# Kernel tuning notes

Measured on AMD Instinct MI355X. Metric: run time of the kernel, lower is better.

## Reference

```python
import jax, jax.numpy as jnp
import numpy as np
from jax import lax

NPOINTS = 1024
K = 32
EPS = 1e-5


def fps(xyz, npoints):
    # Furthest point sampling. xyz: (B, N, 3) -> idx (B, npoints) int32.
    B, N, _ = xyz.shape
    def step(carry, _):
        dists, last = carry
        last_xyz = jnp.take_along_axis(xyz, last[:, None, None], axis=1)  # (B,1,3)
        d = jnp.sum((xyz - last_xyz) ** 2, axis=-1)  # (B,N)
        dists = jnp.minimum(dists, d)
        nxt = jnp.argmax(dists, axis=-1).astype(jnp.int32)
        return (dists, nxt), last
    init = (jnp.full((B, N), 1e10, xyz.dtype), jnp.zeros((B,), jnp.int32))
    _, idx = lax.scan(step, init, None, length=npoints)
    return idx.T  # (B, npoints)


def knn_idx(new_xyz, xyz, k):
    # new_xyz (B,S,3), xyz (B,N,3) -> (B,S,k) indices of k nearest neighbors.
    d = (jnp.sum(new_xyz ** 2, -1)[:, :, None]
         - 2.0 * jnp.einsum('bsc,bnc->bsn', new_xyz, xyz)
         + jnp.sum(xyz ** 2, -1)[:, None, :])  # (B,S,N)
    _, idx = lax.top_k(-d, k)
    return idx


def batch_gather(x, idx):
    # x (B, N, C), idx (B, ...) -> (B, ..., C)
    return jax.vmap(lambda a, i: a[i])(x, idx)


def bn(x, g, b, axes):
    # training-mode batchnorm over `axes`, channel on last axis
    m = jnp.mean(x, axes, keepdims=True)
    v = jnp.var(x, axes, keepdims=True)
    return g * (x - m) * lax.rsqrt(v + EPS) + b


def setup_inputs() -> dict:
    key = jax.random.key(0)
    ks = jax.random.split(key, 8)
    B, N, D, Cw, OUT = 16, 4096, 64, 64, 64
    inp = {
        'xyz': jax.random.uniform(ks[0], (B, N, 3), jnp.float32),
        'feature': jax.random.normal(ks[1], (B, D, N), jnp.float32),
        'w0': jax.random.normal(ks[2], (3, Cw), jnp.float32) * 0.3,
        'b0': jnp.zeros((Cw,), jnp.float32),
        'g0': jnp.ones((Cw,), jnp.float32),
        'be0': jnp.zeros((Cw,), jnp.float32),
        'w1': jax.random.normal(ks[3], (Cw, Cw), jnp.float32) * 0.1,
        'b1': jnp.zeros((Cw,), jnp.float32),
        'g1': jnp.ones((Cw,), jnp.float32),
        'be1': jnp.zeros((Cw,), jnp.float32),
        'w2': jax.random.normal(ks[4], (Cw, Cw), jnp.float32) * 0.1,
        'b2': jnp.zeros((Cw,), jnp.float32),
        'g2': jnp.ones((Cw,), jnp.float32),
        'be2': jnp.zeros((Cw,), jnp.float32),
        'wf': jax.random.normal(ks[5], (D * Cw, OUT), jnp.float32) * 0.02,
        'bf': jnp.zeros((OUT,), jnp.float32),
        'gf': jnp.ones((OUT,), jnp.float32),
        'bef': jnp.zeros((OUT,), jnp.float32),
    }
    return inp


def reference(xyz, feature, w0, b0, g0, be0, w1, b1, g1, be1, w2, b2, g2, be2, wf, bf, gf, bef):
    B, N, _ = xyz.shape
    # FPS + gather centroids
    fps_idx = fps(xyz, NPOINTS)                    # (B, S)
    new_xyz = batch_gather(xyz, fps_idx)           # (B, S, 3)
    # kNN grouping
    idx = knn_idx(new_xyz, xyz, K)                 # (B, S, K)
    grouped_xyz = batch_gather(xyz, idx) - new_xyz[:, :, None, :]   # (B,S,K,3)
    feat_nlast = jnp.swapaxes(feature, 1, 2)       # (B, N, D)
    grouped_feature = batch_gather(feat_nlast, idx)  # (B, S, K, D)
    # WeightNet: 1x1 conv MLP 3 -> Cw -> Cw -> Cw with BN+ReLU
    h = grouped_xyz
    for w, b, g, be in ((w0, b0, g0, be0), (w1, b1, g1, be1), (w2, b2, g2, be2)):
        h = jax.nn.relu(bn(h @ w + b, g, be, (0, 1, 2)))  # (B,S,K,Cw)
    weights = h
    # per-centroid matmul: (B,S,D,K) x (B,S,K,Cw) -> (B,S,D,Cw)
    nf = jnp.einsum('bskd,bskw->bsdw', grouped_feature, weights)
    nf = nf.reshape(B, NPOINTS, -1)                # (B, S, D*Cw)
    # final Conv1d(1x1) + BN1d + ReLU
    out = jax.nn.relu(bn(nf @ wf + bf, gf, bef, (0, 1)))  # (B, S, OUT)
    out = jnp.swapaxes(out, 1, 2)                  # (B, OUT, S)
    return (new_xyz, out)
```

## Files before the change

### kernel.cpp

```cpp
#include <hip/hip_runtime.h>

#define NBATCH 16
#define NPTS   4096
#define NSAMP  1024
#define NKNN   32
#define NROWS  (NBATCH*NSAMP*NKNN)
#define BN_EPS 1e-5f
#define H1PAD  66
#define KNN_CAP 512

typedef __attribute__((ext_vector_type(4))) float f32x4;
typedef __attribute__((ext_vector_type(8))) short bf16x8;
union frag_u { unsigned u[4]; bf16x8 h; uint4 u4; };

__device__ __forceinline__ unsigned pack_bf16pair(float a, float b) {
    unsigned ua = __float_as_uint(a); ua += 0x7FFFu + ((ua >> 16) & 1u);
    unsigned ub = __float_as_uint(b); ub += 0x7FFFu + ((ub >> 16) & 1u);
    return (ua >> 16) | (ub & 0xFFFF0000u);
}

__global__ __launch_bounds__(256) void fps_kernel(const float* __restrict__ xyz,
                                                  float* __restrict__ newxyz)
{
    const int b = blockIdx.x;
    const int tid = threadIdx.x;
    const int wv = tid >> 6;
    const float* xb = xyz + (size_t)b * NPTS * 3;
    __shared__ float xs[NPTS];
    __shared__ float ys[NPTS];
    __shared__ float zs[NPTS];
    __shared__ __align__(16) float4 red[2][4];
    __shared__ __align__(16) float nxs[NSAMP*3];
    float px[16], py[16], pz[16], dmin[16];
    {
        float arr[48];
        const float4* s4 = (const float4*)(xb + (size_t)tid * 48);
        #pragma unroll
        for (int i = 0; i < 12; ++i) *(float4*)&arr[i*4] = s4[i];
        #pragma unroll
        for (int j = 0; j < 16; ++j) {
            px[j] = arr[3*j]; py[j] = arr[3*j+1]; pz[j] = arr[3*j+2];
            const int p = tid * 16 + j;
            xs[p] = px[j]; ys[p] = py[j]; zs[p] = pz[j];
            dmin[j] = 1e10f;
        }
    }
    if (tid == 0) { nxs[0] = xb[0]; nxs[1] = xb[1]; nxs[2] = xb[2]; }
    __syncthreads();
    float lx = xs[0], ly = ys[0], lz = zs[0];
    for (int t = 1; t < NSAMP; ++t) {
        float bv = -1.0f;
        #pragma unroll
        for (int j = 0; j < 16; ++j) {
            const float dx = __fsub_rn(px[j], lx);
            const float dy = __fsub_rn(py[j], ly);
            const float dz = __fsub_rn(pz[j], lz);
            const float d = __fadd_rn(__fadd_rn(__fmul_rn(dx,dx), __fmul_rn(dy,dy)), __fmul_rn(dz,dz));
            const float nd = fminf(dmin[j], d);
            dmin[j] = nd;
            bv = fmaxf(bv, nd);
        }
        int lj = 0;
        #pragma unroll
        for (int j = 15; j >= 0; --j) if (dmin[j] == bv) lj = j;
        const int bi_lane = tid * 16 + lj;
        float mv = bv;
        {
            int s_;
            s_ = __builtin_amdgcn_mov_dpp(__float_as_int(mv), 0x111, 0xf, 0xf, true);
            mv = fmaxf(mv, __int_as_float(s_));
            s_ = __builtin_amdgcn_mov_dpp(__float_as_int(mv), 0x112, 0xf, 0xf, true);
            mv = fmaxf(mv, __int_as_float(s_));
            s_ = __builtin_amdgcn_mov_dpp(__float_as_int(mv), 0x114, 0xf, 0xf, true);
            mv = fmaxf(mv, __int_as_float(s_));
            s_ = __builtin_amdgcn_mov_dpp(__float_as_int(mv), 0x118, 0xf, 0xf, true);
            mv = fmaxf(mv, __int_as_float(s_));
            s_ = __builtin_amdgcn_mov_dpp(__float_as_int(mv), 0x142, 0xf, 0xf, true);
            mv = fmaxf(mv, __int_as_float(s_));
            s_ = __builtin_amdgcn_mov_dpp(__float_as_int(mv), 0x143, 0xf, 0xf, true);
            mv = fmaxf(mv, __int_as_float(s_));
        }
        mv = __int_as_float(__builtin_amdgcn_readlane(__float_as_int(mv), 63));
        const unsigned long long mask = __ballot(bv == mv);
        const int winner = __ffsll(mask) - 1;
        const int bi_w = __builtin_amdgcn_readlane(bi_lane, winner);
        const float wx = xs[bi_w], wy = ys[bi_w], wz = zs[bi_w];
        const int par = t & 1;
        if ((tid & 63) == 0) red[par][wv] = make_float4(mv, wx, wy, wz);
        __syncthreads();
        float4 w0 = red[par][0];
        const float4 w1 = red[par][1];
        const float4 w2 = red[par][2];
        const float4 w3 = red[par][3];
        if (w1.x > w0.x) w0 = w1;
        if (w2.x > w0.x) w0 = w2;
        if (w3.x > w0.x) w0 = w3;
        lx = w0.y; ly = w0.z; lz = w0.w;
        if (tid == 0) { nxs[t*3] = lx; nxs[t*3+1] = ly; nxs[t*3+2] = lz; }
    }
    __syncthreads();
    {
        float4* d4 = (float4*)(newxyz + (size_t)b * NSAMP * 3);
        const float4* s4 = (const float4*)nxs;
        #pragma unroll
        for (int i = tid; i < NSAMP*3/4; i += 256) d4[i] = s4[i];
    }
}

__device__ __forceinline__ void bin_select(int* hist, int* ctrl, int* wsum,
                                           int tid, int shift)
{
    const int lane = tid & 63, wv = tid >> 6;
    const int cnt = hist[tid];
    const int r = ctrl[1];
    int incl = cnt;
    #pragma unroll
    for (int d = 1; d < 64; d <<= 1) {
        const int v = __shfl_up(incl, d);
        if (lane >= d) incl += v;
    }
    if (lane == 63) wsum[wv] = incl;
    __syncthreads();
    int base = 0;
    if (wv > 0) base += wsum[0];
    if (wv > 1) base += wsum[1];
    if (wv > 2) base += wsum[2];
    incl += base;
    const int excl = incl - cnt;
    if (excl < r && r <= incl) {
        ctrl[0] |= tid << shift;
        ctrl[1] = r - excl;
        ctrl[2] = cnt;
    }
}

__global__ __launch_bounds__(256) void knn_kernel(const float* __restrict__ xyz,
                                                  const float* __restrict__ newxyz,
                                                  int* __restrict__ idx_out)
{
    const int bs = blockIdx.x;
    const int b = bs >> 10;
    const int tid = threadIdx.x;
    __shared__ unsigned keys[NPTS];
    __shared__ int hist[256];
    __shared__ float qsh[3];
    __shared__ int ctrl[8];
    __shared__ int wsum[4];
    __shared__ int cl[KNN_CAP];
    __shared__ int lt[32];
    __shared__ int ties[128];
    if (tid < 3) qsh[tid] = newxyz[bs*3 + tid];
    if (tid == 0) { ctrl[0] = 0; ctrl[1] = NKNN; }
    hist[tid] = 0;
    __syncthreads();
    const float q0 = qsh[0], q1 = qsh[1], q2 = qsh[2];
    const float qq = __fadd_rn(__fadd_rn(__fmul_rn(q0,q0), __fmul_rn(q1,q1)), __fmul_rn(q2,q2));
    const float* xb = xyz + (size_t)b * NPTS * 3;
    for (int n = tid; n < NPTS; n += 256) {
        const float x0 = xb[n*3+0], x1 = xb[n*3+1], x2 = xb[n*3+2];
        const float xx = __fadd_rn(__fadd_rn(__fmul_rn(x0,x0), __fmul_rn(x1,x1)), __fmul_rn(x2,x2));
        float dt = __fmul_rn(q0, x0);
        dt = __fmaf_rn(q1, x1, dt);
        dt = __fmaf_rn(q2, x2, dt);
        const float dd = __fadd_rn(__fsub_rn(qq, __fmul_rn(2.0f, dt)), xx);
        unsigned ub = __float_as_uint(dd);
        ub = (ub & 0x80000000u) ? ~ub : (ub | 0x80000000u);
        keys[n] = ub;
        atomicAdd(&hist[ub >> 24], 1);
    }
    __syncthreads();
    bin_select(hist, ctrl, wsum, tid, 24);
    __syncthreads();
    const unsigned pf3 = (unsigned)ctrl[0];
    const int bin3 = (int)(pf3 >> 24);
    const int m = ctrl[2];
    const bool compact = (m <= KNN_CAP);
    if (tid == 0) { ctrl[3] = 0; ctrl[4] = 0; ctrl[5] = 0; ctrl[6] = 0; }
    __syncthreads();
    if (compact) {
        for (int n = tid; n < NPTS; n += 256) {
            const int tb = (int)(keys[n] >> 24);
            if (tb == bin3)      { const int pos = atomicAdd(&ctrl[3], 1); cl[pos] = n; }
            else if (tb < bin3)  { const int pos = atomicAdd(&ctrl[4], 1); lt[pos] = n; }
        }
    }
    __syncthreads();
    for (int p = 2; p >= 0; --p) {
        hist[tid] = 0;
        __syncthreads();
        const unsigned pre = (unsigned)ctrl[0];
        const int shift = p * 8;
        const unsigned himask = 0xFFFFFFFFu << ((p + 1) * 8);
        if (compact) {
            const int eqn = ctrl[3];
            for (int i = tid; i < eqn; i += 256) {
                const unsigned k = keys[cl[i]];
                if ((k & himask) == pre) atomicAdd(&hist[(k >> shift) & 255], 1);
            }
        } else {
            for (int n = tid; n < NPTS; n += 256) {
                const unsigned k = keys[n];
                if ((k & himask) == pre) atomicAdd(&hist[(k >> shift) & 255], 1);
            }
        }
        __syncthreads();
        bin_select(hist, ctrl, wsum, tid, shift);
        __syncthreads();
    }
    const unsigned T = (unsigned)ctrl[0];
    int* out = idx_out + (size_t)bs * NKNN;
    if (compact) {
        const int ltn = ctrl[4];
        if (tid == 0) ctrl[5] = ltn;
        __syncthreads();
        if (tid < ltn) out[tid] = lt[tid];
        const int eqn = ctrl[3];
        for (int i = tid; i < eqn; i += 256) {
            const int n = cl[i];
            const unsigned k = keys[n];
            if (k < T) {
                const int pos = atomicAdd(&ctrl[5], 1);
                if (pos < NKNN) out[pos] = n;
            } else if (k == T) {
                const int pos = atomicAdd(&ctrl[6], 1);
                if (pos < 128) ties[pos] = n;
            }
        }
    } else {
        for (int n = tid; n < NPTS; n += 256) {
            const unsigned k = keys[n];
            if (k < T) {
                const int pos = atomicAdd(&ctrl[5], 1);
                if (pos < NKNN) out[pos] = n;
            } else if (k == T) {
                const int pos = atomicAdd(&ctrl[6], 1);
                if (pos < 128) ties[pos] = n;
            }
        }
    }
    __syncthreads();
    if (tid == 0) {
        const int nless = ctrl[5] < NKNN ? ctrl[5] : NKNN;
        const int need = NKNN - nless;
        const int ntie = ctrl[6] < 128 ? ctrl[6] : 128;
        int last = -1;
        for (int j = 0; j < need; ++j) {
            int best = 0x7fffffff;
            for (int i = 0; i < ntie; ++i) {
                const int v = ties[i];
                if (v > last && v < best) best = v;
            }
            out[nless + j] = (best == 0x7fffffff) ? 0 : best;
            last = best;
        }
    }
}

__global__ void zero_all_kernel(double* st, float* g1, float* g2)
{
    const int i = blockIdx.x * 256 + threadIdx.x;
    if (i < 512) st[i] = 0.0;
    if (i < 4096) { g1[i] = 0.f; g2[i] = 0.f; }
}

__global__ __launch_bounds__(256) void gxmoments_kernel(
    const float* __restrict__ xyz, const float* __restrict__ newxyz,
    const int* __restrict__ idxws, double* __restrict__ stats)
{
    const int tid = threadIdx.x;
    float m[9];
    #pragma unroll
    for (int i = 0; i < 9; ++i) m[i] = 0.f;
    for (int row = blockIdx.x * 256 + tid; row < NROWS; row += gridDim.x * 256) {
        const int bs = row >> 5;
        const int bb = row >> 15;
        const int id = idxws[row];
        const float* xp = xyz + ((size_t)bb * NPTS + id) * 3;
        const float* qp = newxyz + bs * 3;
        const float dx = xp[0] - qp[0];
        const float dy = xp[1] - qp[1];
        const float dz = xp[2] - qp[2];
        m[0] += dx; m[1] += dy; m[2] += dz;
        m[3] += dx*dx; m[4] += dx*dy; m[5] += dx*dz;
        m[6] += dy*dy; m[7] += dy*dz; m[8] += dz*dz;
    }
    double d[9];
    #pragma unroll
    for (int i = 0; i < 9; ++i) {
        d[i] = (double)m[i];
        #pragma unroll
        for (int s = 1; s < 64; s <<= 1) d[i] += __shfl_xor(d[i], s);
    }
    __shared__ double part[4][9];
    if ((tid & 63) == 0) {
        #pragma unroll
        for (int i = 0; i < 9; ++i) part[tid >> 6][i] = d[i];
    }
    __syncthreads();
    if (tid < 9) atomicAdd(&stats[tid], part[0][tid] + part[1][tid] + part[2][tid] + part[3][tid]);
}

__global__ void bn0_moments_finalize_kernel(const double* __restrict__ st,
    const float* __restrict__ w0, const float* __restrict__ b0,
    const float* __restrict__ g0, const float* __restrict__ be0,
    float* __restrict__ outp)
{
    const int c = threadIdx.x;
    const double N = (double)NROWS;
    const double w0c = w0[c], w1c = w0[64 + c], w2c = w0[128 + c];
    const double b = b0[c];
    const double dotS = st[0]*w0c + st[1]*w1c + st[2]*w2c;
    const double qf = w0c*w0c*st[3] + w1c*w1c*st[6] + w2c*w2c*st[8]
                    + 2.0*(w0c*w1c*st[4] + w0c*w2c*st[5] + w1c*w2c*st[7]);
    const double mean = dotS / N + b;
    const double ex2 = (qf + 2.0*b*dotS) / N + b*b;
    const double var = ex2 - mean*mean;
    const float scale = g0[c] * rsqrtf((float)var + BN_EPS);
    outp[c] = scale;
    outp[64 + c] = be0[c] - (float)mean * scale;
}

__global__ void wfpack_all_kernel(const float* __restrict__ wf,
                                  const float* __restrict__ w1,
                                  const float* __restrict__ w2,
                                  unsigned* __restrict__ wfb,
                                  unsigned* __restrict__ w1b,
                                  unsigned* __restrict__ w2b)
{
    int blk = blockIdx.x;
    const float* src; unsigned* dst;
    if (blk < 512)      { src = wf; dst = wfb; }
    else if (blk < 520) { src = w1; dst = w1b; blk -= 512; }
    else                { src = w2; dst = w2b; blk -= 520; }
    const int kt = blk >> 2, ot = blk & 3;
    const int l = threadIdx.x;
    const int o = ot*16 + (l & 15);
    const int kb = kt*32 + (l >> 4)*8;
    unsigned out[4];
    #pragma unroll
    for (int r = 0; r < 4; ++r) {
        const float a = src[(size_t)(kb + 2*r) * 64 + o];
        const float b = src[(size_t)(kb + 2*r + 1) * 64 + o];
        out[r] = pack_bf16pair(a, b);
    }
    *(uint4*)&dst[((size_t)blk * 64 + l) * 4] = *(const uint4*)out;
}

__global__ __launch_bounds__(256) void gram1_kernel(
    const float* __restrict__ xyz, const float* __restrict__ newxyz,
    const int* __restrict__ idxws,
    const float* __restrict__ w0, const float* __restrict__ b0,
    const float* __restrict__ bnp, float* __restrict__ G1,
    double* __restrict__ Sh1)
{
    __shared__ float gxs[32][3];
    __shared__ float h1s[32][H1PAD];
    __shared__ float rsum[256];
    const int tid = threadIdx.x;
    const int c = tid & 63;
    const int rq = tid >> 6;
    const int lg = c >> 4, lm = c & 15;
    const float w0c0 = w0[c], w0c1 = w0[64+c], w0c2 = w0[128+c];
    const float b0c = b0[c], sc0 = bnp[c], sh0 = bnp[64+c];
    f32x4 Ga[4] = {{0,0,0,0},{0,0,0,0},{0,0,0,0},{0,0,0,0}};
    float sumh = 0.f;
    for (int chunk = blockIdx.x; chunk < NROWS/32; chunk += gridDim.x) {
        if (tid < 96) {
            const int slot = tid / 3, cc = tid % 3;
            const int row = chunk*32 + slot;
            const int bs = row >> 5, bb = row >> 15;
            gxs[slot][cc] = xyz[((size_t)bb * NPTS + idxws[row]) * 3 + cc] - newxyz[bs*3 + cc];
        }
        __syncthreads();
        #pragma unroll
        for (int i = 0; i < 8; ++i) {
            const int r = rq*8 + i;
            const float t0 = gxs[r][0]*w0c0 + gxs[r][1]*w0c1 + gxs[r][2]*w0c2 + b0c;
            const float h = fmaxf(sc0*t0 + sh0, 0.f);
            h1s[r][c] = h;
            sumh += h;
        }
        __syncthreads();
        frag_u fr[4];
        #pragma unroll
        for (int ct = 0; ct < 4; ++ct)
            #pragma unroll
            for (int r = 0; r < 4; ++r)
                fr[ct].u[r] = pack_bf16pair(h1s[lg*8 + 2*r][ct*16 + lm],
                                            h1s[lg*8 + 2*r + 1][ct*16 + lm]);
        #pragma unroll
        for (int ct = 0; ct < 4; ++ct)
            Ga[ct] = __builtin_amdgcn_mfma_f32_16x16x32_bf16(fr[rq].h, fr[ct].h, Ga[ct], 0, 0, 0);
        __syncthreads();
    }
    #pragma unroll
    for (int ct = 0; ct < 4; ++ct)
        #pragma unroll
        for (int r = 0; r < 4; ++r)
            atomicAdd(&G1[(rq*16 + lg*4 + r)*64 + ct*16 + lm], Ga[ct][r]);
    rsum[tid] = sumh;
    __syncthreads();
    if (tid < 64) atomicAdd(&Sh1[c], (double)(rsum[c] + rsum[64+c] + rsum[128+c] + rsum[192+c]));
}

__global__ __launch_bounds__(256) void gram2_kernel(
    const float* __restrict__ xyz, const float* __restrict__ newxyz,
    const int* __restrict__ idxws,
    const float* __restrict__ w0, const float* __restrict__ b0,
    const float* __restrict__ b1, const unsigned* __restrict__ w1b,
    const float* __restrict__ bnp, float* __restrict__ G2,
    double* __restrict__ Sh2)
{
    __shared__ float gxs[32][3];
    __shared__ float h1s[32][H1PAD];
    __shared__ float h2s[32][H1PAD];
    __shared__ float rsum[256];
    const int tid = threadIdx.x;
    const int c = tid & 63;
    const int rq = tid >> 6;
    const int lg = c >> 4, lm = c & 15;
    const int c2 = rq*16 + lm;
    const float w0c0 = w0[c], w0c1 = w0[64+c], w0c2 = w0[128+c];
    const float b0c = b0[c], sc0 = bnp[c], sh0 = bnp[64+c];
    const float b1c2 = b1[c2], sc1 = bnp[128+c2], sh1 = bnp[192+c2];
    frag_u Bw1[2];
    Bw1[0].u4 = *(const uint4*)&w1b[((0*4 + rq)*64 + c)*4];
    Bw1[1].u4 = *(const uint4*)&w1b[((1*4 + rq)*64 + c)*4];
    f32x4 Ga[4] = {{0,0,0,0},{0,0,0,0},{0,0,0,0},{0,0,0,0}};
    float sumh = 0.f;
    for (int chunk = blockIdx.x; chunk < NROWS/32; chunk += gridDim.x) {
        if (tid < 96) {
            const int slot = tid / 3, cc = tid % 3;
            const int row = chunk*32 + slot;
            const int bs = row >> 5, bb = row >> 15;
            gxs[slot][cc] = xyz[((size_t)bb * NPTS + idxws[row]) * 3 + cc] - newxyz[bs*3 + cc];
        }
        __syncthreads();
        #pragma unroll
        for (int i = 0; i < 8; ++i) {
            const int r = rq*8 + i;
            const float t0 = gxs[r][0]*w0c0 + gxs[r][1]*w0c1 + gxs[r][2]*w0c2 + b0c;
            h1s[r][c] = fmaxf(sc0*t0 + sh0, 0.f);
        }
        __syncthreads();
        #pragma unroll
        for (int mt = 0; mt < 2; ++mt) {
            f32x4 acc = {0,0,0,0};
            #pragma unroll
            for (int kt = 0; kt < 2; ++kt) {
                frag_u a;
                #pragma unroll
                for (int r = 0; r < 4; ++r) {
                    const float2 f = *(const float2*)&h1s[mt*16 + lm][kt*32 + lg*8 + 2*r];
                    a.u[r] = pack_bf16pair(f.x, f.y);
                }
                acc = __builtin_amdgcn_mfma_f32_16x16x32_bf16(a.h, Bw1[kt].h, acc, 0, 0, 0);
            }
            #pragma unroll
            for (int r = 0; r < 4; ++r)
                h2s[mt*16 + lg*4 + r][c2] = fmaxf(sc1*(acc[r] + b1c2) + sh1, 0.f);
        }
        __syncthreads();
        #pragma unroll
        for (int i = 0; i < 8; ++i) sumh += h2s[rq*8 + i][c];
        frag_u fr[4];
        #pragma unroll
        for (int ct = 0; ct < 4; ++ct)
            #pragma unroll
            for (int r = 0; r < 4; ++r)
                fr[ct].u[r] = pack_bf16pair(h2s[lg*8 + 2*r][ct*16 + lm],
                                            h2s[lg*8 + 2*r + 1][ct*16 + lm]);
        #pragma unroll
        for (int ct = 0; ct < 4; ++ct)
            Ga[ct] = __builtin_amdgcn_mfma_f32_16x16x32_bf16(fr[rq].h, fr[ct].h, Ga[ct], 0, 0, 0);
        __syncthreads();
    }
    #pragma unroll
    for (int ct = 0; ct < 4; ++ct)
        #pragma unroll
        for (int r = 0; r < 4; ++r)
            atomicAdd(&G2[(rq*16 + lg*4 + r)*64 + ct*16 + lm], Ga[ct][r]);
    rsum[tid] = sumh;
    __syncthreads();
    if (tid < 64) atomicAdd(&Sh2[c], (double)(rsum[c] + rsum[64+c] + rsum[128+c] + rsum[192+c]));
}

__global__ __launch_bounds__(256) void bn_gram_finalize_kernel(
    const double* __restrict__ Sh, const float* __restrict__ G,
    const float* __restrict__ w, const float* __restrict__ bias,
    const float* __restrict__ g, const float* __restrict__ be,
    float* __restrict__ outp)
{
    __shared__ float wls[64][65];
    __shared__ double shl[64];
    __shared__ double rd[256], rqd[256];
    const int tid = threadIdx.x;
    const int c = tid & 63;
    const int rqi = tid >> 6;
    for (int i = tid; i < 4096; i += 256) wls[i >> 6][i & 63] = w[i];
    if (tid < 64) shl[tid] = Sh[tid];
    __syncthreads();
    double dot = 0.0, quad = 0.0;
    for (int j = rqi*16; j < rqi*16 + 16; ++j) {
        const double wjc = (double)wls[j][c];
        dot += wjc * shl[j];
        double inner = 0.0;
        for (int k = 0; k < 64; ++k) inner += (double)G[j*64 + k] * (double)wls[k][c];
        quad += wjc * inner;
    }
    rd[tid] = dot; rqd[tid] = quad;
    __syncthreads();
    if (tid < 64) {
        const double d = rd[c] + rd[64+c] + rd[128+c] + rd[192+c];
        const double q = rqd[c] + rqd[64+c] + rqd[128+c] + rqd[192+c];
        const double N = (double)NROWS;
        const double bc = (double)bias[c];
        const double mean = d / N + bc;
        const double ex2 = (q + 2.0*bc*d) / N + bc*bc;
        const double var = ex2 - mean*mean;
        const float scale = g[c] * rsqrtf((float)var + BN_EPS);
        outp[c] = scale;
        outp[64 + c] = be[c] - (float)mean * scale;
    }
}

__global__ void bn_finalize_kernel(const double* __restrict__ st,
                                   const float* __restrict__ g,
                                   const float* __restrict__ be,
                                   float* __restrict__ outp, float n)
{
    const int c = threadIdx.x;
    const double m = st[c] / (double)n;
    const double var = st[64 + c] / (double)n - m * m;
    const float scale = g[c] * rsqrtf((float)var + BN_EPS);
    outp[c] = scale;
    outp[64 + c] = be[c] - (float)m * scale;
}

__global__ __launch_bounds__(256) void final_conv_kernel(
    const float* __restrict__ xyz, const float* __restrict__ newxyz,
    const int* __restrict__ idxws, const float* __restrict__ feat,
    const float* __restrict__ w0, const float* __restrict__ b0,
    const float* __restrict__ b1, const float* __restrict__ b2,
    const float* __restrict__ bnp, const unsigned* __restrict__ wfb,
    const unsigned* __restrict__ w1b, const unsigned* __restrict__ w2b,
    const float* __restrict__ bf, float* __restrict__ y)
{
    __shared__ unsigned wtp[8][16][64];
    __shared__ __align__(16) float scratch[2*64*H1PAD];
    __shared__ float gxs[256][3];
    __shared__ int   idxs[8][32];
    __shared__ float qs[8][3];
    float* h1s = scratch;
    float* h2s = scratch + 64*H1PAD;
    unsigned* yaf = (unsigned*)scratch;
    const int tid = threadIdx.x;
    const int c = tid & 63;
    const int rq = tid >> 6;
    const int lg = c >> 4, lm = c & 15;
    const int c2 = rq*16 + lm;
    const int bs0 = blockIdx.x * 8;
    const int b = bs0 >> 10;
    idxs[tid >> 5][tid & 31] = idxws[(size_t)bs0 * NKNN + tid];
    if (tid < 24)  qs[tid / 3][tid % 3] = newxyz[(bs0 + tid/3)*3 + (tid % 3)];
    const float w0c0 = w0[c], w0c1 = w0[64+c], w0c2 = w0[128+c];
    const float b0c = b0[c], sc0 = bnp[c], sh0 = bnp[64+c];
    const float b1c2 = b1[c2], sc1 = bnp[128+c2], sh1 = bnp[192+c2];
    const float b2c2 = b2[c2], sc2 = bnp[256+c2], sh2 = bnp[320+c2];
    frag_u Bw1[2], Bw2[2];
    #pragma unroll
    for (int kt = 0; kt < 2; ++kt) {
        Bw1[kt].u4 = *(const uint4*)&w1b[((kt*4 + rq)*64 + c)*4];
        Bw2[kt].u4 = *(const uint4*)&w2b[((kt*4 + rq)*64 + c)*4];
    }
    __syncthreads();
    for (int i = tid; i < 768; i += 256) {
        const int row = i / 3, cc = i - row * 3;
        const int e = row >> 5, k = row & 31;
        gxs[row][cc] = xyz[((size_t)b * NPTS + idxs[e][k]) * 3 + cc] - qs[e][cc];
    }
    __syncthreads();
    for (int chunk = 0; chunk < 4; ++chunk) {
        #pragma unroll
        for (int i = 0; i < 16; ++i) {
            const int r = rq*16 + i;
            const int gr = chunk*64 + r;
            const float t0 = gxs[gr][0]*w0c0 + gxs[gr][1]*w0c1 + gxs[gr][2]*w0c2 + b0c;
            h1s[r*H1PAD + c] = fmaxf(sc0*t0 + sh0, 0.f);
        }
        __syncthreads();
        #pragma unroll
        for (int mt = 0; mt < 4; ++mt) {
            f32x4 acc = {0,0,0,0};
            #pragma unroll
            for (int kt = 0; kt < 2; ++kt) {
                frag_u a;
                #pragma unroll
                for (int r = 0; r < 4; ++r) {
                    const float2 f = *(const float2*)&h1s[(mt*16 + lm)*H1PAD + kt*32 + lg*8 + 2*r];
                    a.u[r] = pack_bf16pair(f.x, f.y);
                }
                acc = __builtin_amdgcn_mfma_f32_16x16x32_bf16(a.h, Bw1[kt].h, acc, 0, 0, 0);
            }
            #pragma unroll
            for (int r = 0; r < 4; ++r)
                h2s[(mt*16 + lg*4 + r)*H1PAD + c2] = fmaxf(sc1*(acc[r] + b1c2) + sh1, 0.f);
        }
        __syncthreads();
        #pragma unroll
        for (int mt = 0; mt < 4; ++mt) {
            f32x4 acc = {0,0,0,0};
            #pragma unroll
            for (int kt = 0; kt < 2; ++kt) {
                frag_u a;
                #pragma unroll
                for (int r = 0; r < 4; ++r) {
                    const float2 f = *(const float2*)&h2s[(mt*16 + lm)*H1PAD + kt*32 + lg*8 + 2*r];
                    a.u[r] = pack_bf16pair(f.x, f.y);
                }
                acc = __builtin_amdgcn_mfma_f32_16x16x32_bf16(a.h, Bw2[kt].h, acc, 0, 0, 0);
            }
            float wt[4];
            #pragma unroll
            for (int r = 0; r < 4; ++r)
                wt[r] = fmaxf(sc2*(acc[r] + b2c2) + sh2, 0.f);
            const int grow0 = chunk*64 + mt*16 + lg*4;
            const int e = grow0 >> 5, kl = grow0 & 31;
            wtp[e][kl >> 1][c2]       = pack_bf16pair(wt[0], wt[1]);
            wtp[e][(kl >> 1) + 1][c2] = pack_bf16pair(wt[2], wt[3]);
        }
        __syncthreads();
    }
    const int lane = c;
    const int wid = rq;
    frag_u afr[2][4];
    #pragma unroll
    for (int es = 0; es < 2; ++es)
        #pragma unroll
        for (int w4 = 0; w4 < 4; ++w4)
            #pragma unroll
            for (int r = 0; r < 4; ++r)
                afr[es][w4].u[r] = wtp[wid*2 + es][lg*4 + r][w4*16 + lm];
    f32x4 yaccA = {0.f, 0.f, 0.f, 0.f};
    f32x4 yaccB = {0.f, 0.f, 0.f, 0.f};
    for (int dhalf = 0; dhalf < 2; ++dhalf) {
        #pragma unroll
        for (int es = 0; es < 2; ++es) {
            const int e = wid*2 + es;
            #pragma unroll
            for (int dt = 0; dt < 2; ++dt) {
                const int d = dhalf*32 + dt*16 + lm;
                const float* fb = feat + (size_t)(b*64 + d) * NPTS;
                frag_u B;
                #pragma unroll
                for (int r = 0; r < 4; ++r) {
                    const int k0 = lg*8 + 2*r;
                    B.u[r] = pack_bf16pair(fb[idxs[e][k0]], fb[idxs[e][k0+1]]);
                }
                #pragma unroll
                for (int w4 = 0; w4 < 4; ++w4) {
                    f32x4 dnf = {0.f, 0.f, 0.f, 0.f};
                    dnf = __builtin_amdgcn_mfma_f32_16x16x32_bf16(afr[es][w4].h, B.h, dnf, 0, 0, 0);
                    const unsigned p0 = pack_bf16pair(dnf[0], dnf[1]);
                    const unsigned p1 = pack_bf16pair(dnf[2], dnf[3]);
                    const int dloc = dt*16 + lm;
                    const int kp0 = dloc*32 + w4*8 + lg*2;
                    const int sw = kp0 ^ ((lm & 3) << 3) ^ ((e & 7) << 2);
                    *(uint2*)&yaf[e*1024 + sw] = make_uint2(p0, p1);
                }
            }
        }
        __syncthreads();
        for (int kt = 0; kt < 64; kt += 2) {
            frag_u A0, B0, A1, B1;
            const int kpb0 = (kt*16 + lg*4) ^ (((kt >> 1) & 3) << 3) ^ ((lm & 7) << 2);
            const int kpb1 = ((kt+1)*16 + lg*4) ^ ((((kt+1) >> 1) & 3) << 3) ^ ((lm & 7) << 2);
            A0.u4 = *(const uint4*)&yaf[(lm & 7)*1024 + kpb0];
            A1.u4 = *(const uint4*)&yaf[(lm & 7)*1024 + kpb1];
            B0.u4 = *(const uint4*)&wfb[(((size_t)(dhalf*64 + kt)*4 + wid)*64 + lane)*4];
            B1.u4 = *(const uint4*)&wfb[(((size_t)(dhalf*64 + kt + 1)*4 + wid)*64 + lane)*4];
            yaccA = __builtin_amdgcn_mfma_f32_16x16x32_bf16(A0.h, B0.h, yaccA, 0, 0, 0);
            yaccB = __builtin_amdgcn_mfma_f32_16x16x32_bf16(A1.h, B1.h, yaccB, 0, 0, 0);
        }
        __syncthreads();
    }
    if (lg < 2) {
        const float bfo = bf[wid*16 + lm];
        #pragma unroll
        for (int r = 0; r < 4; ++r)
            y[(size_t)(bs0 + lg*4 + r) * 64 + wid*16 + lm] = (yaccA[r] + yaccB[r]) + bfo;
    }
}

__global__ __launch_bounds__(256) void ystats_kernel(const float* __restrict__ y,
                                                     double* __restrict__ st)
{
    const int tid = threadIdx.x;
    const int c = tid & 63;
    double s = 0.0, s2 = 0.0;
    for (int i = blockIdx.x * 256 + tid; i < NBATCH*NSAMP*64; i += gridDim.x * 256) {
        const float v = y[i];
        s += v; s2 += (double)v * (double)v;
    }
    __shared__ double rs[256], rs2[256];
    rs[tid] = s; rs2[tid] = s2;
    __syncthreads();
    if (tid < 64) {
        const double a  = rs[c]  + rs[64+c]  + rs[128+c]  + rs[192+c];
        const double a2 = rs2[c] + rs2[64+c] + rs2[128+c] + rs2[192+c];
        atomicAdd(&st[c], a);
        atomicAdd(&st[64 + c], a2);
    }
}

__global__ void writeout_kernel(const float* __restrict__ y,
                                const float* __restrict__ bnp3,
                                float* __restrict__ outp)
{
    const int i = blockIdx.x * 256 + threadIdx.x;
    if (i >= NBATCH * 64 * NSAMP) return;
    const int s = i & 1023;
    const int o = (i >> 10) & 63;
    const int bb = i >> 16;
    const float v = y[((size_t)(bb << 10) + s) * 64 + o];
    outp[i] = fmaxf(bnp3[o] * v + bnp3[64 + o], 0.f);
}

extern "C" void kernel_launch(void* const* d_in, const int* in_sizes, int n_in,
                              void* d_out, int out_size, void* d_ws, size_t ws_size,
                              hipStream_t stream)
{
    (void)in_sizes; (void)n_in; (void)out_size; (void)ws_size;
    const float* xyz  = (const float*)d_in[0];
    const float* feat = (const float*)d_in[1];
    const float* w0   = (const float*)d_in[2];
    const float* b0   = (const float*)d_in[3];
    const float* g0   = (const float*)d_in[4];
    const float* be0  = (const float*)d_in[5];
    const float* w1   = (const float*)d_in[6];
    const float* b1   = (const float*)d_in[7];
    const float* g1   = (const float*)d_in[8];
    const float* be1  = (const float*)d_in[9];
    const float* w2   = (const float*)d_in[10];
    const float* b2   = (const float*)d_in[11];
    const float* g2   = (const float*)d_in[12];
    const float* be2  = (const float*)d_in[13];
    const float* wf   = (const float*)d_in[14];
    const float* bf   = (const float*)d_in[15];
    const float* gf   = (const float*)d_in[16];
    const float* bef  = (const float*)d_in[17];

    float* out = (float*)d_out;
    float* newxyz = out;
    float* outmain = out + NBATCH * NSAMP * 3;

    char* ws = (char*)d_ws;
    int*      idxws = (int*)ws;
    float*    ybuf  = (float*)(ws + 2097152);
    double*   stats = (double*)(ws + 6291456);
    float*    bnp   = (float*)(ws + 6295552);
    unsigned* wfb   = (unsigned*)(ws + 6297600);
    unsigned* w1b   = (unsigned*)(ws + 6821888);
    unsigned* w2b   = (unsigned*)(ws + 6830080);
    float*    G1    = (float*)(ws + 6838272);
    float*    G2    = (float*)(ws + 6854656);

    zero_all_kernel<<<16, 256, 0, stream>>>(stats, G1, G2);
    wfpack_all_kernel<<<528, 64, 0, stream>>>(wf, w1, w2, wfb, w1b, w2b);
    fps_kernel<<<NBATCH, 256, 0, stream>>>(xyz, newxyz);
    knn_kernel<<<NBATCH * NSAMP, 256, 0, stream>>>(xyz, newxyz, idxws);

    gxmoments_kernel<<<1024, 256, 0, stream>>>(xyz, newxyz, idxws, stats);
    bn0_moments_finalize_kernel<<<1, 64, 0, stream>>>(stats, w0, b0, g0, be0, bnp);
    gram1_kernel<<<256, 256, 0, stream>>>(xyz, newxyz, idxws, w0, b0, bnp, G1, stats + 128);
    bn_gram_finalize_kernel<<<1, 256, 0, stream>>>(stats + 128, G1, w1, b1, g1, be1, bnp + 128);
    gram2_kernel<<<256, 256, 0, stream>>>(xyz, newxyz, idxws, w0, b0, b1, w1b, bnp, G2, stats + 192);
    bn_gram_finalize_kernel<<<1, 256, 0, stream>>>(stats + 192, G2, w2, b2, g2, be2, bnp + 256);

    final_conv_kernel<<<NBATCH * NSAMP / 8, 256, 0, stream>>>(
        xyz, newxyz, idxws, feat, w0, b0, b1, b2, bnp, wfb, w1b, w2b, bf, ybuf);

    ystats_kernel<<<256, 256, 0, stream>>>(ybuf, stats + 384);
    bn_finalize_kernel<<<1, 64, 0, stream>>>(stats + 384, gf, bef, bnp + 384, (float)(NBATCH * NSAMP));
    writeout_kernel<<<4096, 256, 0, stream>>>(ybuf, bnp + 384, outmain);
}
```

Baseline: 1.396 ms.

## Pre-transpose features to bf16, cache grouped xyz, and aggregate histogram atomics

Adds a kernel that transposes the feature tensor to a point-major bf16 layout, so the final conv gathers contiguous channels per neighbor instead of strided fp32 loads. gxmoments now writes the relative grouped xyz to workspace, and gram1, gram2 and final_conv read it instead of re-gathering it from xyz. The kNN histogram uses wave-level ballot aggregation to cut LDS atomic contention. In exchange it adds an extra transpose pass and more workspace traffic, and the ballot loop may serialise when bins are diverse.

```diff
diff --git a/kernel.cpp b/kernel.cpp
--- a/kernel.cpp
+++ b/kernel.cpp
@@ -17,6 +17,10 @@
     unsigned ua = __float_as_uint(a); ua += 0x7FFFu + ((ua >> 16) & 1u);
     unsigned ub = __float_as_uint(b); ub += 0x7FFFu + ((ub >> 16) & 1u);
     return (ua >> 16) | (ub & 0xFFFF0000u);
+}
+__device__ __forceinline__ unsigned short bf16_rne(float a) {
+    unsigned ua = __float_as_uint(a); ua += 0x7FFFu + ((ua >> 16) & 1u);
+    return (unsigned short)(ua >> 16);
 }
 
 __global__ __launch_bounds__(256) void fps_kernel(const float* __restrict__ xyz,
@@ -141,6 +145,7 @@
     const int bs = blockIdx.x;
     const int b = bs >> 10;
     const int tid = threadIdx.x;
+    const int lane = tid & 63;
     __shared__ unsigned keys[NPTS];
     __shared__ int hist[256];
     __shared__ float qsh[3];
@@ -166,7 +171,15 @@
         unsigned ub = __float_as_uint(dd);
         ub = (ub & 0x80000000u) ? ~ub : (ub | 0x80000000u);
         keys[n] = ub;
-        atomicAdd(&hist[ub >> 24], 1);
+        const int bin = (int)(ub >> 24);
+        unsigned long long act = __ballot(true);
+        while (act) {
+            const int leader = __ffsll(act) - 1;
+            const int lbin = __builtin_amdgcn_readlane(bin, leader);
+            const unsigned long long same = __ballot(bin == lbin);
+            if (lane == leader) atomicAdd(&hist[lbin], (int)__popcll(same));
+            act &= ~same;
+        }
     }
     __syncthreads();
     bin_select(hist, ctrl, wsum, tid, 24);
@@ -256,6 +269,28 @@
     }
 }
 
+__global__ __launch_bounds__(256) void feat_transpose_kernel(
+    const float* __restrict__ feat, unsigned short* __restrict__ tfeat)
+{
+    __shared__ unsigned short t[64][65];
+    const int blk = blockIdx.x;
+    const int b = blk >> 6, nt = blk & 63;
+    const int tid = threadIdx.x;
+    #pragma unroll
+    for (int i = 0; i < 16; ++i) {
+        const int e = i*256 + tid;
+        const int d = e >> 6, n = e & 63;
+        t[n][d] = bf16_rne(feat[((size_t)(b*64 + d))*NPTS + nt*64 + n]);
+    }
+    __syncthreads();
+    #pragma unroll
+    for (int i = 0; i < 16; ++i) {
+        const int e = i*256 + tid;
+        const int n = e >> 6, d = e & 63;
+        tfeat[((size_t)(b*NPTS) + nt*64 + n)*64 + d] = t[n][d];
+    }
+}
+
 __global__ void zero_all_kernel(double* st, float* g1, float* g2)
 {
     const int i = blockIdx.x * 256 + threadIdx.x;
@@ -265,7 +300,8 @@
 
 __global__ __launch_bounds__(256) void gxmoments_kernel(
     const float* __restrict__ xyz, const float* __restrict__ newxyz,
-    const int* __restrict__ idxws, double* __restrict__ stats)
+    const int* __restrict__ idxws, double* __restrict__ stats,
+    float* __restrict__ gxws)
 {
     const int tid = threadIdx.x;
     float m[9];
@@ -280,6 +316,9 @@
         const float dx = xp[0] - qp[0];
         const float dy = xp[1] - qp[1];
         const float dz = xp[2] - qp[2];
+        gxws[(size_t)row*3 + 0] = dx;
+        gxws[(size_t)row*3 + 1] = dy;
+        gxws[(size_t)row*3 + 2] = dz;
         m[0] += dx; m[1] += dy; m[2] += dz;
         m[3] += dx*dx; m[4] += dx*dy; m[5] += dx*dz;
         m[6] += dy*dy; m[7] += dy*dz; m[8] += dz*dz;
@@ -347,8 +386,7 @@
 }
 
 __global__ __launch_bounds__(256) void gram1_kernel(
-    const float* __restrict__ xyz, const float* __restrict__ newxyz,
-    const int* __restrict__ idxws,
+    const float* __restrict__ gxws,
     const float* __restrict__ w0, const float* __restrict__ b0,
     const float* __restrict__ bnp, float* __restrict__ G1,
     double* __restrict__ Sh1)
@@ -365,12 +403,7 @@
     f32x4 Ga[4] = {{0,0,0,0},{0,0,0,0},{0,0,0,0},{0,0,0,0}};
     float sumh = 0.f;
     for (int chunk = blockIdx.x; chunk < NROWS/32; chunk += gridDim.x) {
-        if (tid < 96) {
-            const int slot = tid / 3, cc = tid % 3;
-            const int row = chunk*32 + slot;
-            const int bs = row >> 5, bb = row >> 15;
-            gxs[slot][cc] = xyz[((size_t)bb * NPTS + idxws[row]) * 3 + cc] - newxyz[bs*3 + cc];
-        }
+        if (tid < 96) ((float*)gxs)[tid] = gxws[(size_t)chunk*96 + tid];
         __syncthreads();
         #pragma unroll
         for (int i = 0; i < 8; ++i) {
@@ -404,8 +437,7 @@
 }
 
 __global__ __launch_bounds__(256) void gram2_kernel(
-    const float* __restrict__ xyz, const float* __restrict__ newxyz,
-    const int* __restrict__ idxws,
+    const float* __restrict__ gxws,
     const float* __restrict__ w0, const float* __restrict__ b0,
     const float* __restrict__ b1, const unsigned* __restrict__ w1b,
     const float* __restrict__ bnp, float* __restrict__ G2,
@@ -429,12 +461,7 @@
     f32x4 Ga[4] = {{0,0,0,0},{0,0,0,0},{0,0,0,0},{0,0,0,0}};
     float sumh = 0.f;
     for (int chunk = blockIdx.x; chunk < NROWS/32; chunk += gridDim.x) {
-        if (tid < 96) {
-            const int slot = tid / 3, cc = tid % 3;
-            const int row = chunk*32 + slot;
-            const int bs = row >> 5, bb = row >> 15;
-            gxs[slot][cc] = xyz[((size_t)bb * NPTS + idxws[row]) * 3 + cc] - newxyz[bs*3 + cc];
-        }
+        if (tid < 96) ((float*)gxs)[tid] = gxws[(size_t)chunk*96 + tid];
         __syncthreads();
         #pragma unroll
         for (int i = 0; i < 8; ++i) {
@@ -538,8 +565,8 @@
 }
 
 __global__ __launch_bounds__(256) void final_conv_kernel(
-    const float* __restrict__ xyz, const float* __restrict__ newxyz,
-    const int* __restrict__ idxws, const float* __restrict__ feat,
+    const float* __restrict__ gxws,
+    const int* __restrict__ idxws, const unsigned short* __restrict__ tfeat,
     const float* __restrict__ w0, const float* __restrict__ b0,
     const float* __restrict__ b1, const float* __restrict__ b2,
     const float* __restrict__ bnp, const unsigned* __restrict__ wfb,
@@ -550,7 +577,6 @@
     __shared__ __align__(16) float scratch[2*64*H1PAD];
     __shared__ float gxs[256][3];
     __shared__ int   idxs[8][32];
-    __shared__ float qs[8][3];
     float* h1s = scratch;
     float* h2s = scratch + 64*H1PAD;
     unsigned* yaf = (unsigned*)scratch;
@@ -562,7 +588,6 @@
     const int bs0 = blockIdx.x * 8;
     const int b = bs0 >> 10;
     idxs[tid >> 5][tid & 31] = idxws[(size_t)bs0 * NKNN + tid];
-    if (tid < 24)  qs[tid / 3][tid % 3] = newxyz[(bs0 + tid/3)*3 + (tid % 3)];
     const float w0c0 = w0[c], w0c1 = w0[64+c], w0c2 = w0[128+c];
     const float b0c = b0[c], sc0 = bnp[c], sh0 = bnp[64+c];
     const float b1c2 = b1[c2], sc1 = bnp[128+c2], sh1 = bnp[192+c2];
@@ -573,12 +598,8 @@
         Bw1[kt].u4 = *(const uint4*)&w1b[((kt*4 + rq)*64 + c)*4];
         Bw2[kt].u4 = *(const uint4*)&w2b[((kt*4 + rq)*64 + c)*4];
     }
-    __syncthreads();
-    for (int i = tid; i < 768; i += 256) {
-        const int row = i / 3, cc = i - row * 3;
-        const int e = row >> 5, k = row & 31;
-        gxs[row][cc] = xyz[((size_t)b * NPTS + idxs[e][k]) * 3 + cc] - qs[e][cc];
-    }
+    for (int i = tid; i < 768; i += 256)
+        ((float*)gxs)[i] = gxws[(size_t)bs0*96 + i];
     __syncthreads();
     for (int chunk = 0; chunk < 4; ++chunk) {
         #pragma unroll
@@ -643,6 +664,7 @@
                 afr[es][w4].u[r] = wtp[wid*2 + es][lg*4 + r][w4*16 + lm];
     f32x4 yaccA = {0.f, 0.f, 0.f, 0.f};
     f32x4 yaccB = {0.f, 0.f, 0.f, 0.f};
+    const unsigned short* tfb = tfeat + (size_t)b * NPTS * 64;
     for (int dhalf = 0; dhalf < 2; ++dhalf) {
         #pragma unroll
         for (int es = 0; es < 2; ++es) {
@@ -650,12 +672,13 @@
             #pragma unroll
             for (int dt = 0; dt < 2; ++dt) {
                 const int d = dhalf*32 + dt*16 + lm;
-                const float* fb = feat + (size_t)(b*64 + d) * NPTS;
                 frag_u B;
                 #pragma unroll
                 for (int r = 0; r < 4; ++r) {
                     const int k0 = lg*8 + 2*r;
-                    B.u[r] = pack_bf16pair(fb[idxs[e][k0]], fb[idxs[e][k0+1]]);
+                    const unsigned va = tfb[(size_t)idxs[e][k0]   * 64 + d];
+                    const unsigned vb = tfb[(size_t)idxs[e][k0+1] * 64 + d];
+                    B.u[r] = va | (vb << 16);
                 }
                 #pragma unroll
                 for (int w4 = 0; w4 < 4; ++w4) {
@@ -764,21 +787,24 @@
     unsigned* w2b   = (unsigned*)(ws + 6830080);
     float*    G1    = (float*)(ws + 6838272);
     float*    G2    = (float*)(ws + 6854656);
+    float*    gxws  = (float*)(ws + 6871040);
+    unsigned short* tfeat = (unsigned short*)(ws + 13164544);
 
     zero_all_kernel<<<16, 256, 0, stream>>>(stats, G1, G2);
     wfpack_all_kernel<<<528, 64, 0, stream>>>(wf, w1, w2, wfb, w1b, w2b);
+    feat_transpose_kernel<<<1024, 256, 0, stream>>>(feat, tfeat);
     fps_kernel<<<NBATCH, 256, 0, stream>>>(xyz, newxyz);
     knn_kernel<<<NBATCH * NSAMP, 256, 0, stream>>>(xyz, newxyz, idxws);
 
-    gxmoments_kernel<<<1024, 256, 0, stream>>>(xyz, newxyz, idxws, stats);
+    gxmoments_kernel<<<1024, 256, 0, stream>>>(xyz, newxyz, idxws, stats, gxws);
     bn0_moments_finalize_kernel<<<1, 64, 0, stream>>>(stats, w0, b0, g0, be0, bnp);
-    gram1_kernel<<<256, 256, 0, stream>>>(xyz, newxyz, idxws, w0, b0, bnp, G1, stats + 128);
+    gram1_kernel<<<256, 256, 0, stream>>>(gxws, w0, b0, bnp, G1, stats + 128);
     bn_gram_finalize_kernel<<<1, 256, 0, stream>>>(stats + 128, G1, w1, b1, g1, be1, bnp + 128);
-    gram2_kernel<<<256, 256, 0, stream>>>(xyz, newxyz, idxws, w0, b0, b1, w1b, bnp, G2, stats + 192);
+    gram2_kernel<<<256, 256, 0, stream>>>(gxws, w0, b0, b1, w1b, bnp, G2, stats + 192);
     bn_gram_finalize_kernel<<<1, 256, 0, stream>>>(stats + 192, G2, w2, b2, g2, be2, bnp + 256);
 
     final_conv_kernel<<<NBATCH * NSAMP / 8, 256, 0, stream>>>(
-        xyz, newxyz, idxws, feat, w0, b0, b1, b2, bnp, wfb, w1b, w2b, bf, ybuf);
+        gxws, idxws, tfeat, w0, b0, b1, b2, bnp, wfb, w1b, w2b, bf, ybuf);
 
     ystats_kernel<<<256, 256, 0, stream>>>(ybuf, stats + 384);
     bn_finalize_kernel<<<1, 64, 0, stream>>>(stats + 384, gf, bef, bnp + 384, (float)(NBATCH * NSAMP));
```

Result: faster. 1.236 ms (-11.5%).
